# Performance work log

Measured on AMD Instinct MI355X. Metric: run time of the kernel, lower is better.

Reference implementation:

```python
import jax, jax.numpy as jnp
import numpy as np

N, M, IN, H, OUT, L = 100000, 50000, 256, 256, 128, 2
E_RAND = 150000  # extra random incidences beyond coverage prefixes
GN_STRUCT_EPS = float(H)  # GraphNorm(hidden, hidden): 2nd positional arg is eps!


def _l2n(a):
    return a / jnp.maximum(jnp.linalg.norm(a, axis=1, keepdims=True), 1e-12)


def _ln(x, g, b, eps=1e-5):
    m = x.mean(-1, keepdims=True)
    v = ((x - m) ** 2).mean(-1, keepdims=True)
    return (x - m) / jnp.sqrt(v + eps) * g + b


def _gn(x, w, b, ms, eps):
    # PyG GraphNorm with batch=None (single graph)
    mean = x.mean(0, keepdims=True)
    out = x - mean * ms
    var = (out ** 2).mean(0, keepdims=True)
    return w * out / jnp.sqrt(var + eps) + b


def _hgconv(xn, W, bias, src, dst, n_nodes, n_edges):
    # PyG HypergraphConv, use_attention=False -> heads=1, lin has no bias
    xw = xn @ W.T                                                # [n_nodes, H]
    ones = jnp.ones(src.shape[0], xw.dtype)
    Dn = jax.ops.segment_sum(ones, src, num_segments=n_nodes)   # node degree
    Dn = jnp.where(Dn > 0, 1.0 / Dn, 0.0)
    Be = jax.ops.segment_sum(ones, dst, num_segments=n_edges)   # hyperedge degree
    Be = jnp.where(Be > 0, 1.0 / Be, 0.0)
    he = jax.ops.segment_sum(xw[src], dst, num_segments=n_edges) * Be[:, None]
    out = jax.ops.segment_sum(he[dst], src, num_segments=n_nodes) * Dn[:, None]
    return out + bias


def _forward(x, x_e, x_struct_table, w_in, b_in, w_e, b_e, w_sem, b_sem,
             ln_n_g, ln_n_b, hg_w, hg_b,
             gn_struct_w, gn_struct_b, gn_struct_ms,
             gn_llm_w, gn_llm_b, gn_llm_ms,
             gn_d_w, gn_d_b, gn_d_ms,
             skip_w, skip_b,
             nf_ln1_g, nf_ln1_b, nf_w, nf_b, nf_ln2_g, nf_ln2_b,
             ef_ln1_g, ef_ln1_b, ef_w, ef_b, ef_ln2_g, ef_ln2_b,
             lin_w, lin_b, edge_index):
    lrelu = jax.nn.leaky_relu  # slope 0.01 == nn.LeakyReLU default
    src, dst = edge_index[0], edge_index[1]
    n, m = x.shape[0], x_e.shape[0]
    # edge_index[0] covers all nodes, so unique(edge_index[0]) == arange(N)
    xs = lrelu(_l2n(x_struct_table) @ w_in.T + b_in)   # dropout: eval mode (identity)
    xn = lrelu(_l2n(x) @ w_sem.T + b_sem)
    xe = lrelu(_l2n(x_e) @ w_e.T + b_e)
    for i in range(L):
        xs = _ln(xs, ln_n_g[i], ln_n_b[i])
        xs = lrelu(_hgconv(xs, hg_w[i, 0], hg_b[i, 0], src, dst, n, m)) + \
             _gn(xs, gn_struct_w[i], gn_struct_b[i], gn_struct_ms[i], GN_STRUCT_EPS)
        xn = _gn(xn, gn_llm_w[i], gn_llm_b[i], gn_llm_ms[i], 1e-5)
        xn = lrelu(_hgconv(xn, hg_w[i, 1], hg_b[i, 1], src, dst, n, m)) + \
             (xn @ skip_w[i, 0].T + skip_b[i, 0])
        agg = jax.ops.segment_min(xn[src], dst, num_segments=m)  # MinAggregation
        xe = _gn(xe + agg, gn_d_w[i], gn_d_b[i], gn_d_ms[i], 1e-5)
        # dual hypergraph: hyperedges become nodes (flip of edge_index)
        xe = lrelu(_hgconv(xe, hg_w[i, 2], hg_b[i, 2], dst, src, m, n)) + \
             (xe @ skip_w[i, 1].T + skip_b[i, 1])
    xf = jnp.concatenate([xs, xn], axis=1)
    xf = _ln(xf, nf_ln1_g, nf_ln1_b)
    xf = lrelu(xf @ nf_w.T + nf_b)
    xf = _ln(xf, nf_ln2_g, nf_ln2_b)
    xa = jax.ops.segment_min(xf[src], dst, num_segments=m)
    xef = jnp.concatenate([xa, xe], axis=1)
    xef = _ln(xef, ef_ln1_g, ef_ln1_b)
    xef = lrelu(xef @ ef_w.T + ef_b)
    xef = _ln(xef, ef_ln2_g, ef_ln2_b)
    return xef @ lin_w.T + lin_b  # [M, OUT]


def setup_inputs() -> dict:
    key = jax.random.key(0)
    ks = iter(jax.random.split(key, 64))
    def nrm(shape, scale=0.05):
        return jax.random.normal(next(ks), shape, dtype=jnp.float32) * scale
    # incidence list with guaranteed coverage of all nodes and all hyperedges
    src = jnp.concatenate([jnp.arange(N),
                           jax.random.randint(next(ks), (M + E_RAND,), 0, N)])
    dst = jnp.concatenate([jax.random.randint(next(ks), (N,), 0, M),
                           jnp.arange(M),
                           jax.random.randint(next(ks), (E_RAND,), 0, M)])
    edge_index = jnp.stack([src, dst]).astype(jnp.int32)  # [2, 300000]
    return dict(
        x=nrm((N, IN), 1.0), x_e=nrm((M, IN), 1.0), x_struct_table=nrm((N, IN), 1.0),
        w_in=nrm((H, IN)), b_in=jnp.zeros((H,)),
        w_e=nrm((H, IN)), b_e=jnp.zeros((H,)),
        w_sem=nrm((H, IN)), b_sem=jnp.zeros((H,)),
        ln_n_g=jnp.ones((L, H)), ln_n_b=jnp.zeros((L, H)),
        hg_w=nrm((L, 3, H, H)), hg_b=jnp.zeros((L, 3, H)),
        gn_struct_w=jnp.ones((L, H)), gn_struct_b=jnp.zeros((L, H)), gn_struct_ms=jnp.ones((L, H)),
        gn_llm_w=jnp.ones((L, H)), gn_llm_b=jnp.zeros((L, H)), gn_llm_ms=jnp.ones((L, H)),
        gn_d_w=jnp.ones((L, H)), gn_d_b=jnp.zeros((L, H)), gn_d_ms=jnp.ones((L, H)),
        skip_w=nrm((L, 2, H, H)), skip_b=jnp.zeros((L, 2, H)),
        nf_ln1_g=jnp.ones((2 * H,)), nf_ln1_b=jnp.zeros((2 * H,)),
        nf_w=nrm((H, 2 * H)), nf_b=jnp.zeros((H,)),
        nf_ln2_g=jnp.ones((H,)), nf_ln2_b=jnp.zeros((H,)),
        ef_ln1_g=jnp.ones((2 * H,)), ef_ln1_b=jnp.zeros((2 * H,)),
        ef_w=nrm((H, 2 * H)), ef_b=jnp.zeros((H,)),
        ef_ln2_g=jnp.ones((H,)), ef_ln2_b=jnp.zeros((H,)),
        lin_w=nrm((OUT, H)), lin_b=jnp.zeros((OUT,)),
        edge_index=edge_index,
    )


def reference(x, x_e, x_struct_table, w_in, b_in, w_e, b_e, w_sem, b_sem,
              ln_n_g, ln_n_b, hg_w, hg_b,
              gn_struct_w, gn_struct_b, gn_struct_ms,
              gn_llm_w, gn_llm_b, gn_llm_ms,
              gn_d_w, gn_d_b, gn_d_ms,
              skip_w, skip_b,
              nf_ln1_g, nf_ln1_b, nf_w, nf_b, nf_ln2_g, nf_ln2_b,
              ef_ln1_g, ef_ln1_b, ef_w, ef_b, ef_ln2_g, ef_ln2_b,
              lin_w, lin_b, edge_index):
    return _forward(x, x_e, x_struct_table, w_in, b_in, w_e, b_e, w_sem, b_sem,
                    ln_n_g, ln_n_b, hg_w, hg_b,
                    gn_struct_w, gn_struct_b, gn_struct_ms,
                    gn_llm_w, gn_llm_b, gn_llm_ms,
                    gn_d_w, gn_d_b, gn_d_ms,
                    skip_w, skip_b,
                    nf_ln1_g, nf_ln1_b, nf_w, nf_b, nf_ln2_g, nf_ln2_b,
                    ef_ln1_g, ef_ln1_b, ef_w, ef_b, ef_ln2_g, ef_ln2_b,
                    lin_w, lin_b, edge_index)
```

## Files before the change

kernel.cpp:

```cpp
#include <hip/hip_runtime.h>

typedef unsigned short u16;
struct __align__(16) us8 { ushort4 a, b; };
typedef __attribute__((ext_vector_type(8))) short bf16x8;
typedef __attribute__((ext_vector_type(4))) float f32x4;

#define CDIV(a,b) (((a)+(b)-1)/(b))

__device__ __forceinline__ float bf2f(u16 u){ return __uint_as_float(((unsigned)u)<<16); }
__device__ __forceinline__ u16 f2bf(float f){
  unsigned u=__float_as_uint(f);
  unsigned r=u+0x7fffu+((u>>16)&1u);
  return (u16)(r>>16);
}
__device__ __forceinline__ float lrelu_f(float v){ return v>0.f? v:0.01f*v; }
__device__ __forceinline__ float wsum(float v){
  #pragma unroll
  for(int o=32;o>0;o>>=1) v+=__shfl_xor(v,o,64);
  return v;
}
__device__ __forceinline__ void us8_to_f(const us8& v, float* f){
  f[0]=bf2f(v.a.x); f[1]=bf2f(v.a.y); f[2]=bf2f(v.a.z); f[3]=bf2f(v.a.w);
  f[4]=bf2f(v.b.x); f[5]=bf2f(v.b.y); f[6]=bf2f(v.b.z); f[7]=bf2f(v.b.w);
}
__device__ __forceinline__ us8 f_to_us8(const float* f){
  us8 v;
  v.a.x=f2bf(f[0]); v.a.y=f2bf(f[1]); v.a.z=f2bf(f[2]); v.a.w=f2bf(f[3]);
  v.b.x=f2bf(f[4]); v.b.y=f2bf(f[5]); v.b.z=f2bf(f[6]); v.b.w=f2bf(f[7]);
  return v;
}

__global__ void zero_k(unsigned* __restrict__ p, int n){
  int i=blockIdx.x*256+threadIdx.x; if(i<n) p[i]=0u;
}
__global__ void cvt_k(const float* __restrict__ in, u16* __restrict__ out, int n){
  int i = (blockIdx.x*256+threadIdx.x)*4;
  if(i+3<n){
    float4 v=*(const float4*)(in+i);
    ushort4 o; o.x=f2bf(v.x); o.y=f2bf(v.y); o.z=f2bf(v.z); o.w=f2bf(v.w);
    *(ushort4*)(out+i)=o;
  } else {
    for(int q=0;q<4&&i+q<n;q++) out[i+q]=f2bf(in[i+q]);
  }
}

__global__ void count_k(const int* __restrict__ src, const int* __restrict__ dst, int E,
                        int* __restrict__ cnt_src, int* __restrict__ cnt_dst){
  int e = blockIdx.x*256+threadIdx.x;
  if(e>=E) return;
  atomicAdd(&cnt_src[src[e]],1);
  atomicAdd(&cnt_dst[dst[e]],1);
}

#define SCAN_CHUNK 1024
__global__ void scan_pass1(const int* __restrict__ in, int n, int* __restrict__ partial){
  __shared__ int red[256];
  int base = blockIdx.x*SCAN_CHUNK;
  int s=0;
  for(int j=threadIdx.x;j<SCAN_CHUNK;j+=256){ int i=base+j; if(i<n) s+=in[i]; }
  red[threadIdx.x]=s; __syncthreads();
  for(int st=128;st>0;st>>=1){ if(threadIdx.x<st) red[threadIdx.x]+=red[threadIdx.x+st]; __syncthreads(); }
  if(threadIdx.x==0) partial[blockIdx.x]=red[0];
}
__global__ void scan_pass2(int* __restrict__ partial, int nb){
  __shared__ int buf[1024];
  for(int j=threadIdx.x;j<1024;j+=256) buf[j] = (j<nb)? partial[j]:0;
  __syncthreads();
  if(threadIdx.x==0){ int run=0; for(int j=0;j<nb;j++){ int v=buf[j]; buf[j]=run; run+=v; } }
  __syncthreads();
  for(int j=threadIdx.x;j<nb;j+=256) partial[j]=buf[j];
}
__global__ void scan_pass3(const int* __restrict__ in, int n, const int* __restrict__ partial,
                           int* __restrict__ out, int total){
  __shared__ int red[256];
  int base = blockIdx.x*SCAN_CHUNK;
  int j0 = base + threadIdx.x*4;
  int v[4]; int s=0;
  #pragma unroll
  for(int q=0;q<4;q++){ int i=j0+q; v[q]=(i<n)? in[i]:0; s+=v[q]; }
  red[threadIdx.x]=s; __syncthreads();
  if(threadIdx.x==0){ int run=0; for(int j=0;j<256;j++){ int t=red[j]; red[j]=run; run+=t; } }
  __syncthreads();
  int run = partial[blockIdx.x] + red[threadIdx.x];
  #pragma unroll
  for(int q=0;q<4;q++){ int i=j0+q; if(i<n) out[i]=run; run+=v[q]; }
  if(base==0 && threadIdx.x==0) out[n]=total;
}
__global__ void copy_int_k(const int* __restrict__ in, int* __restrict__ out, int n){
  int i=blockIdx.x*256+threadIdx.x;
  if(i<n) out[i]=in[i];
}
__global__ void fill_adj_k(const int* __restrict__ src, const int* __restrict__ dst, int E,
                           int* __restrict__ cur_src, int* __restrict__ cur_dst,
                           int* __restrict__ adj_sd, int* __restrict__ adj_ds){
  int e = blockIdx.x*256+threadIdx.x;
  if(e>=E) return;
  int s=src[e], d=dst[e];
  int p = atomicAdd(&cur_dst[d],1); adj_ds[p]=s;
  int q = atomicAdd(&cur_src[s],1); adj_sd[q]=d;
}
__global__ void invdeg_k(const int* __restrict__ off, float* __restrict__ inv, int S){
  int s=blockIdx.x*256+threadIdx.x;
  if(s>=S) return;
  int d=off[s+1]-off[s];
  inv[s] = d>0 ? 1.0f/(float)d : 0.0f;
}

__global__ void l2norm_k(const float* __restrict__ in, u16* __restrict__ out, int R){
  int r = blockIdx.x*4 + (threadIdx.x>>6);
  if(r>=R) return;
  int c = (threadIdx.x&63)*4;
  float4 v = *(const float4*)(in + (size_t)r*256 + c);
  float q = wsum(v.x*v.x+v.y*v.y+v.z*v.z+v.w*v.w);
  float sc = 1.0f/fmaxf(sqrtf(q),1e-12f);
  ushort4 o; o.x=f2bf(v.x*sc); o.y=f2bf(v.y*sc); o.z=f2bf(v.z*sc); o.w=f2bf(v.w*sc);
  *(ushort4*)(out + (size_t)r*256 + c) = o;
}

__global__ void ln_rows_k(u16* __restrict__ x, const float* __restrict__ g,
                          const float* __restrict__ b, int R){
  int r = blockIdx.x*4 + (threadIdx.x>>6);
  if(r>=R) return;
  int lane = threadIdx.x&63; int c = lane*4;
  u16* row = x + (size_t)r*256;
  ushort4 u = *(const ushort4*)(row + c);
  float v0=bf2f(u.x), v1=bf2f(u.y), v2=bf2f(u.z), v3=bf2f(u.w);
  float mean = wsum(v0+v1+v2+v3) * (1.f/256.f);
  float d0=v0-mean,d1=v1-mean,d2=v2-mean,d3=v3-mean;
  float var = wsum(d0*d0+d1*d1+d2*d2+d3*d3) * (1.f/256.f);
  float inv = 1.0f/sqrtf(var + 1e-5f);
  ushort4 ov;
  ov.x=f2bf(d0*inv*g[c+0]+b[c+0]);
  ov.y=f2bf(d1*inv*g[c+1]+b[c+1]);
  ov.z=f2bf(d2*inv*g[c+2]+b[c+2]);
  ov.w=f2bf(d3*inv*g[c+3]+b[c+3]);
  *(ushort4*)(row + c) = ov;
}

__global__ void ln512_k(u16* __restrict__ Lb, u16* __restrict__ Rb,
                        const float* __restrict__ g, const float* __restrict__ b, int R){
  int r = blockIdx.x*4 + (threadIdx.x>>6);
  if(r>=R) return;
  int lane = threadIdx.x&63; int c = lane*4;
  u16* rowL = Lb + (size_t)r*256;
  u16* rowR = Rb + (size_t)r*256;
  ushort4 ul = *(const ushort4*)(rowL + c);
  ushort4 ur = *(const ushort4*)(rowR + c);
  float l0=bf2f(ul.x), l1=bf2f(ul.y), l2=bf2f(ul.z), l3=bf2f(ul.w);
  float r0=bf2f(ur.x), r1=bf2f(ur.y), r2=bf2f(ur.z), r3=bf2f(ur.w);
  float mean = wsum(l0+l1+l2+l3+r0+r1+r2+r3) * (1.f/512.f);
  float a0=l0-mean,a1=l1-mean,a2=l2-mean,a3=l3-mean;
  float b0=r0-mean,b1=r1-mean,b2=r2-mean,b3=r3-mean;
  float var = wsum(a0*a0+a1*a1+a2*a2+a3*a3+b0*b0+b1*b1+b2*b2+b3*b3) * (1.f/512.f);
  float inv = 1.0f/sqrtf(var + 1e-5f);
  int cr = 256+c;
  ushort4 ovl, ovr;
  ovl.x=f2bf(a0*inv*g[c+0]+b[c+0]);
  ovl.y=f2bf(a1*inv*g[c+1]+b[c+1]);
  ovl.z=f2bf(a2*inv*g[c+2]+b[c+2]);
  ovl.w=f2bf(a3*inv*g[c+3]+b[c+3]);
  ovr.x=f2bf(b0*inv*g[cr+0]+b[cr+0]);
  ovr.y=f2bf(b1*inv*g[cr+1]+b[cr+1]);
  ovr.z=f2bf(b2*inv*g[cr+2]+b[cr+2]);
  ovr.w=f2bf(b3*inv*g[cr+3]+b[cr+3]);
  *(ushort4*)(rowL + c) = ovl;
  *(ushort4*)(rowR + c) = ovr;
}

__global__ void colstat_k(const u16* __restrict__ x, const u16* __restrict__ x2,
                          float* __restrict__ stat, int R){
  __shared__ float sh[512];
  int tid = threadIdx.x;
  for(int j=tid;j<512;j+=256) sh[j]=0.f;
  __syncthreads();
  int c = (tid&63)*4;
  float s0=0,s1=0,s2=0,s3=0,q0=0,q1=0,q2=0,q3=0;
  for(int r=blockIdx.x*4+(tid>>6); r<R; r+=gridDim.x*4){
    ushort4 u = *(const ushort4*)(x + (size_t)r*256 + c);
    float v0=bf2f(u.x), v1=bf2f(u.y), v2=bf2f(u.z), v3=bf2f(u.w);
    if(x2){
      ushort4 w = *(const ushort4*)(x2 + (size_t)r*256 + c);
      v0+=bf2f(w.x); v1+=bf2f(w.y); v2+=bf2f(w.z); v3+=bf2f(w.w);
    }
    s0+=v0; s1+=v1; s2+=v2; s3+=v3;
    q0+=v0*v0; q1+=v1*v1; q2+=v2*v2; q3+=v3*v3;
  }
  atomicAdd(&sh[c+0],s0); atomicAdd(&sh[c+1],s1);
  atomicAdd(&sh[c+2],s2); atomicAdd(&sh[c+3],s3);
  atomicAdd(&sh[256+c+0],q0); atomicAdd(&sh[256+c+1],q1);
  atomicAdd(&sh[256+c+2],q2); atomicAdd(&sh[256+c+3],q3);
  __syncthreads();
  for(int j=tid;j<512;j+=256) atomicAdd(&stat[j], sh[j]);
}
__global__ void gn_final_k(const float* __restrict__ stat, const float* __restrict__ w,
                           const float* __restrict__ b, const float* __restrict__ ms,
                           float eps, float invR,
                           float* __restrict__ gA, float* __restrict__ gS, float* __restrict__ gB){
  int c=threadIdx.x;
  float mean = stat[c]*invR;
  float a = mean*ms[c];
  float ex2 = stat[256+c]*invR;
  float var = ex2 - 2.f*a*mean + a*a;
  gA[c]=a;
  gS[c]=w[c]/sqrtf(var+eps);
  gB[c]=b[c];
}
__global__ void apply_gn_k(u16* __restrict__ x, const u16* __restrict__ add,
                           const float* __restrict__ gA, const float* __restrict__ gS,
                           const float* __restrict__ gB, size_t n4){
  size_t stride = (size_t)gridDim.x*256;
  for(size_t p=(size_t)blockIdx.x*256+threadIdx.x; p<n4; p+=stride){
    int c = (int)(p&63)*4;
    ushort4 u = ((const ushort4*)x)[p];
    float v0=bf2f(u.x), v1=bf2f(u.y), v2=bf2f(u.z), v3=bf2f(u.w);
    if(add){
      ushort4 a = ((const ushort4*)add)[p];
      v0+=bf2f(a.x); v1+=bf2f(a.y); v2+=bf2f(a.z); v3+=bf2f(a.w);
    }
    v0 = fmaf(gS[c+0], v0-gA[c+0], gB[c+0]);
    v1 = fmaf(gS[c+1], v1-gA[c+1], gB[c+1]);
    v2 = fmaf(gS[c+2], v2-gA[c+2], gB[c+2]);
    v3 = fmaf(gS[c+3], v3-gA[c+3], gB[c+3]);
    ushort4 o; o.x=f2bf(v0); o.y=f2bf(v1); o.z=f2bf(v2); o.w=f2bf(v3);
    ((ushort4*)x)[p]=o;
  }
}

template<int MODE>
__global__ void seg_sum_k(const u16* __restrict__ in, u16* __restrict__ out,
    const int* __restrict__ adj, const int* __restrict__ off,
    const float* __restrict__ inv, const float* __restrict__ bias,
    const u16* __restrict__ resid,
    const float* __restrict__ gA, const float* __restrict__ gS, const float* __restrict__ gB,
    int S){
  int s = blockIdx.x*8 + (threadIdx.x>>5);
  if(s>=S) return;
  int c = (threadIdx.x&31)*8;
  int jb=off[s], je=off[s+1];
  float a[8]={0.f,0.f,0.f,0.f,0.f,0.f,0.f,0.f};
  for(int j=jb;j<je;j++){
    us8 v = *(const us8*)(in + (size_t)adj[j]*256 + c);
    float f[8]; us8_to_f(v,f);
    #pragma unroll
    for(int q=0;q<8;q++) a[q]+=f[q];
  }
  float sc = inv[s];
  float o[8];
  if(MODE==0){
    #pragma unroll
    for(int q=0;q<8;q++) o[q]=a[q]*sc;
  } else {
    #pragma unroll
    for(int q=0;q<8;q++) o[q] = lrelu_f(fmaf(a[q],sc,bias[c+q]));
    us8 p = *(const us8*)(resid + (size_t)s*256 + c);
    float pf[8]; us8_to_f(p,pf);
    if(MODE==1){
      #pragma unroll
      for(int q=0;q<8;q++) o[q] += fmaf(gS[c+q], pf[q]-gA[c+q], gB[c+q]);
    } else {
      #pragma unroll
      for(int q=0;q<8;q++) o[q] += pf[q];
    }
  }
  *(us8*)(out + (size_t)s*256 + c) = f_to_us8(o);
}

__global__ void seg_min_k(const u16* __restrict__ in, u16* __restrict__ out,
    const int* __restrict__ adj, const int* __restrict__ off, int S){
  int s = blockIdx.x*8 + (threadIdx.x>>5);
  if(s>=S) return;
  int c = (threadIdx.x&31)*8;
  int jb=off[s], je=off[s+1];
  float m[8];
  #pragma unroll
  for(int q=0;q<8;q++) m[q]=3.402823466e38f;
  for(int j=jb;j<je;j++){
    us8 v = *(const us8*)(in + (size_t)adj[j]*256 + c);
    float f[8]; us8_to_f(v,f);
    #pragma unroll
    for(int q=0;q<8;q++) m[q]=fminf(m[q],f[q]);
  }
  if(jb==je){
    #pragma unroll
    for(int q=0;q<8;q++) m[q]=0.f;
  }
  *(us8*)(out + (size_t)s*256 + c) = f_to_us8(m);
}

template<int FLAGS, int JT>
__global__ __launch_bounds__(512, 3)
void gemm_mfma(const u16* A0, const u16* __restrict__ A1,
               const u16* __restrict__ Wb, const float* __restrict__ bias,
               u16* Cb, float* __restrict__ Cf, int R, int K){
  const int CN = JT*64;
  __shared__ u16 sm[64*(JT*64+8)];
  const int t = threadIdx.x;
  const int row0 = blockIdx.x*128;
  const int lane = t&63;
  const int w = t>>6;
  const int wrow = (w>>2)*64, wcol = (w&3)*(JT*16);
  const int lm = lane&15, q = lane>>4;
  f32x4 acc[4][4];
  #pragma unroll
  for(int i=0;i<4;i++)
    #pragma unroll
    for(int j=0;j<JT;j++) acc[i][j] = (f32x4){0.f,0.f,0.f,0.f};

  int arow[4];
  #pragma unroll
  for(int i=0;i<4;i++){
    int r = row0 + wrow + i*16 + lm;
    arow[i] = r < R ? r : (R-1);
  }
  const u16* brow[JT];
  #pragma unroll
  for(int j=0;j<JT;j++) brow[j] = Wb + (size_t)(wcol + j*16 + lm)*K + q*8;

  #pragma unroll 2
  for(int kt=0; kt<K; kt+=32){
    const u16* Ab = ((FLAGS&8) && kt>=256) ? A1 : A0;
    const int kc = (kt & 255) + q*8;
    bf16x8 af[4], bfv[4];
    #pragma unroll
    for(int i=0;i<4;i++)  af[i]  = *(const bf16x8*)(Ab + (size_t)arow[i]*256 + kc);
    #pragma unroll
    for(int j=0;j<JT;j++) bfv[j] = *(const bf16x8*)(brow[j] + kt);
    #pragma unroll
    for(int i=0;i<4;i++)
      #pragma unroll
      for(int j=0;j<JT;j++)
        acc[i][j] = __builtin_amdgcn_mfma_f32_16x16x32_bf16(af[i], bfv[j], acc[i][j], 0,0,0);
  }

  float bvals[4];
  #pragma unroll
  for(int j=0;j<JT;j++) bvals[j] = (FLAGS&1) ? bias[wcol+j*16+lm] : 0.f;

  if(FLAGS&4){
    #pragma unroll
    for(int j=0;j<JT;j++){
      int col = wcol + j*16 + lm;
      #pragma unroll
      for(int i=0;i<4;i++){
        int rbase = row0 + wrow + i*16 + q*4;
        #pragma unroll
        for(int rg=0;rg<4;rg++){
          int r = rbase+rg;
          if(r>=R) continue;
          float v = acc[i][j][rg] + bvals[j];
          if(FLAGS&2) v = lrelu_f(v);
          Cf[(size_t)r*CN+col] = v;
        }
      }
    }
  } else {
    const int CEPI = CN+8;
    const int ROWU = CN/8;
    #pragma unroll
    for(int h=0; h<2; h++){
      if((w>>2)==h){
        #pragma unroll
        for(int j=0;j<JT;j++){
          int cl = wcol + j*16 + lm;
          #pragma unroll
          for(int i=0;i<4;i++){
            #pragma unroll
            for(int rg=0;rg<4;rg++){
              float v = acc[i][j][rg] + bvals[j];
              if(FLAGS&2) v = lrelu_f(v);
              sm[(i*16 + q*4 + rg)*CEPI + cl] = f2bf(v);
            }
          }
        }
      }
      __syncthreads();
      #pragma unroll
      for(int it=0; it<64*ROWU/512; it++){
        int idx = it*512 + t;
        int rl = idx/ROWU, c8 = (idx - rl*ROWU)*8;
        int r = row0 + h*64 + rl;
        if(r<R) *(us8*)(Cb + (size_t)r*CN + c8) = *(const us8*)(&sm[rl*CEPI + c8]);
      }
      __syncthreads();
    }
  }
}

extern "C" void kernel_launch(void* const* d_in, const int* in_sizes, int n_in,
                              void* d_out, int out_size, void* d_ws, size_t ws_size,
                              hipStream_t stream){
  const int H = 256;
  const int N = in_sizes[0]/H;
  const int M = in_sizes[1]/H;
  const int E = in_sizes[38]/2;

  const float* x     = (const float*)d_in[0];
  const float* x_e   = (const float*)d_in[1];
  const float* x_st  = (const float*)d_in[2];
  const float* w_in  = (const float*)d_in[3];  const float* b_in  = (const float*)d_in[4];
  const float* w_e   = (const float*)d_in[5];  const float* b_e   = (const float*)d_in[6];
  const float* w_sem = (const float*)d_in[7];  const float* b_sem = (const float*)d_in[8];
  const float* ln_n_g = (const float*)d_in[9]; const float* ln_n_b = (const float*)d_in[10];
  const float* hg_w  = (const float*)d_in[11]; const float* hg_b  = (const float*)d_in[12];
  const float* gns_w = (const float*)d_in[13]; const float* gns_b = (const float*)d_in[14]; const float* gns_ms = (const float*)d_in[15];
  const float* gnl_w = (const float*)d_in[16]; const float* gnl_b = (const float*)d_in[17]; const float* gnl_ms = (const float*)d_in[18];
  const float* gnd_w = (const float*)d_in[19]; const float* gnd_b = (const float*)d_in[20]; const float* gnd_ms = (const float*)d_in[21];
  const float* skip_w = (const float*)d_in[22]; const float* skip_b = (const float*)d_in[23];
  const float* nf_ln1_g = (const float*)d_in[24]; const float* nf_ln1_b = (const float*)d_in[25];
  const float* nf_w = (const float*)d_in[26]; const float* nf_b = (const float*)d_in[27];
  const float* nf_ln2_g = (const float*)d_in[28]; const float* nf_ln2_b = (const float*)d_in[29];
  const float* ef_ln1_g = (const float*)d_in[30]; const float* ef_ln1_b = (const float*)d_in[31];
  const float* ef_w = (const float*)d_in[32]; const float* ef_b = (const float*)d_in[33];
  const float* ef_ln2_g = (const float*)d_in[34]; const float* ef_ln2_b = (const float*)d_in[35];
  const float* lin_w = (const float*)d_in[36]; const float* lin_b = (const float*)d_in[37];
  const int* edge = (const int*)d_in[38];
  const int* src = edge;
  const int* dst = edge + E;
  float* outp = (float*)d_out;

  const size_t NH=(size_t)N*H, MH=(size_t)M*H;
  u16* XS = (u16*)d_ws;
  u16* XN = XS + NH;
  u16* TN = XN + NH;
  u16* XE = TN + NH;
  u16* TM = XE + MH;
  float* dinv = (float*)(TM + MH);
  float* binv = dinv + N;
  float* stat = binv + M;
  float* gA = stat+512; float* gS = gA+256; float* gB = gS+256;
  int* cnt_src = (int*)(gB+256);
  int* cnt_dst = cnt_src + N;
  int* off_src = cnt_dst + M;
  int* off_dst = off_src + (N+1);
  int* adj_ds = off_dst + (M+1);
  int* adj_sd = adj_ds + E;
  int* partial = adj_sd + E;
  u16* wb = (u16*)(((uintptr_t)(partial+1024)+15)&~(uintptr_t)15);
  u16* wb_in  = wb;
  u16* wb_sem = wb_in  + 65536;
  u16* wb_e   = wb_sem + 65536;
  u16* wb_hg  = wb_e   + 65536;
  u16* wb_sk  = wb_hg  + 6*65536;
  u16* wb_nf  = wb_sk  + 4*65536;
  u16* wb_ef  = wb_nf  + 131072;
  u16* wb_lin = wb_ef  + 131072;

  cvt_k<<<CDIV(65536,1024),256,0,stream>>>(w_in, wb_in, 65536);
  cvt_k<<<CDIV(65536,1024),256,0,stream>>>(w_sem, wb_sem, 65536);
  cvt_k<<<CDIV(65536,1024),256,0,stream>>>(w_e, wb_e, 65536);
  cvt_k<<<CDIV(6*65536,1024),256,0,stream>>>(hg_w, wb_hg, 6*65536);
  cvt_k<<<CDIV(4*65536,1024),256,0,stream>>>(skip_w, wb_sk, 4*65536);
  cvt_k<<<CDIV(131072,1024),256,0,stream>>>(nf_w, wb_nf, 131072);
  cvt_k<<<CDIV(131072,1024),256,0,stream>>>(ef_w, wb_ef, 131072);
  cvt_k<<<CDIV(32768,1024),256,0,stream>>>(lin_w, wb_lin, 32768);

  zero_k<<<CDIV(N+M,256),256,0,stream>>>((unsigned*)cnt_src, N+M);
  count_k<<<CDIV(E,256),256,0,stream>>>(src,dst,E,cnt_src,cnt_dst);
  int nbN = CDIV(N,SCAN_CHUNK), nbM = CDIV(M,SCAN_CHUNK);
  scan_pass1<<<nbN,256,0,stream>>>(cnt_src,N,partial);
  scan_pass2<<<1,256,0,stream>>>(partial,nbN);
  scan_pass3<<<nbN,256,0,stream>>>(cnt_src,N,partial,off_src,E);
  scan_pass1<<<nbM,256,0,stream>>>(cnt_dst,M,partial);
  scan_pass2<<<1,256,0,stream>>>(partial,nbM);
  scan_pass3<<<nbM,256,0,stream>>>(cnt_dst,M,partial,off_dst,E);
  copy_int_k<<<CDIV(N,256),256,0,stream>>>(off_src,cnt_src,N);
  copy_int_k<<<CDIV(M,256),256,0,stream>>>(off_dst,cnt_dst,M);
  fill_adj_k<<<CDIV(E,256),256,0,stream>>>(src,dst,E,cnt_src,cnt_dst,adj_sd,adj_ds);
  invdeg_k<<<CDIV(N,256),256,0,stream>>>(off_src,dinv,N);
  invdeg_k<<<CDIV(M,256),256,0,stream>>>(off_dst,binv,M);

  auto gemm = [&](int F, const u16* A0, const u16* A1, const u16* Wt, const float* bias,
                  u16* Cb, float* Cf, int R, int K){
    dim3 g(CDIV(R,128));
    switch(F){
      case 0:  gemm_mfma<0,4> <<<g,512,0,stream>>>(A0,A1,Wt,bias,Cb,Cf,R,K); break;
      case 1:  gemm_mfma<1,4> <<<g,512,0,stream>>>(A0,A1,Wt,bias,Cb,Cf,R,K); break;
      case 3:  gemm_mfma<3,4> <<<g,512,0,stream>>>(A0,A1,Wt,bias,Cb,Cf,R,K); break;
      case 5:  gemm_mfma<5,2> <<<g,512,0,stream>>>(A0,A1,Wt,bias,Cb,Cf,R,K); break;
      case 11: gemm_mfma<11,4><<<g,512,0,stream>>>(A0,A1,Wt,bias,Cb,Cf,R,K); break;
    }
  };
  auto colstats = [&](const u16* xx, const u16* x2, const float* w, const float* b,
                      const float* ms, float eps, int R){
    zero_k<<<2,256,0,stream>>>((unsigned*)stat, 512);
    colstat_k<<<256,256,0,stream>>>(xx, x2, stat, R);
    gn_final_k<<<1,256,0,stream>>>(stat, w, b, ms, eps, 1.0f/(float)R, gA,gS,gB);
  };

  l2norm_k<<<CDIV(N,4),256,0,stream>>>(x_st, TN, N);
  gemm(3, TN, nullptr, wb_in, b_in, XS, nullptr, N, 256);
  l2norm_k<<<CDIV(N,4),256,0,stream>>>(x, TN, N);
  gemm(3, TN, nullptr, wb_sem, b_sem, XN, nullptr, N, 256);
  l2norm_k<<<CDIV(M,4),256,0,stream>>>(x_e, TM, M);
  gemm(3, TM, nullptr, wb_e, b_e, XE, nullptr, M, 256);

  for(int i=0;i<2;i++){
    ln_rows_k<<<CDIV(N,4),256,0,stream>>>(XS, ln_n_g+i*H, ln_n_b+i*H, N);
    colstats(XS, nullptr, gns_w+i*H, gns_b+i*H, gns_ms+i*H, 256.0f, N);
    seg_sum_k<0><<<CDIV(M,8),256,0,stream>>>(XS, TM, adj_ds, off_dst, binv, nullptr,nullptr,nullptr,nullptr,nullptr, M);
    gemm(0, TM, nullptr, wb_hg+(size_t)(i*3+0)*65536, nullptr, TM, nullptr, M, 256);
    seg_sum_k<1><<<CDIV(N,8),256,0,stream>>>(TM, XS, adj_sd, off_src, dinv, hg_b+(size_t)(i*3+0)*H, XS, gA,gS,gB, N);

    colstats(XN, nullptr, gnl_w+i*H, gnl_b+i*H, gnl_ms+i*H, 1e-5f, N);
    apply_gn_k<<<1024,256,0,stream>>>(XN, nullptr, gA,gS,gB, NH/4);
    seg_sum_k<0><<<CDIV(M,8),256,0,stream>>>(XN, TM, adj_ds, off_dst, binv, nullptr,nullptr,nullptr,nullptr,nullptr, M);
    gemm(0, TM, nullptr, wb_hg+(size_t)(i*3+1)*65536, nullptr, TM, nullptr, M, 256);
    gemm(1, XN, nullptr, wb_sk+(size_t)(i*2+0)*65536, skip_b+(size_t)(i*2+0)*H, TN, nullptr, N, 256);
    seg_sum_k<2><<<CDIV(N,8),256,0,stream>>>(TM, XN, adj_sd, off_src, dinv, hg_b+(size_t)(i*3+1)*H, TN, nullptr,nullptr,nullptr, N);

    seg_min_k<<<CDIV(M,8),256,0,stream>>>(XN, TM, adj_ds, off_dst, M);
    colstats(XE, TM, gnd_w+i*H, gnd_b+i*H, gnd_ms+i*H, 1e-5f, M);
    apply_gn_k<<<1024,256,0,stream>>>(XE, TM, gA,gS,gB, MH/4);
    gemm(0, XE, nullptr, wb_hg+(size_t)(i*3+2)*65536, nullptr, TM, nullptr, M, 256);
    seg_sum_k<0><<<CDIV(N,8),256,0,stream>>>(TM, TN, adj_sd, off_src, dinv, nullptr,nullptr,nullptr,nullptr,nullptr, N);
    gemm(1, XE, nullptr, wb_sk+(size_t)(i*2+1)*65536, skip_b+(size_t)(i*2+1)*H, TM, nullptr, M, 256);
    seg_sum_k<2><<<CDIV(M,8),256,0,stream>>>(TN, XE, adj_ds, off_dst, binv, hg_b+(size_t)(i*3+2)*H, TM, nullptr,nullptr,nullptr, M);
  }

  ln512_k<<<CDIV(N,4),256,0,stream>>>(XS, XN, nf_ln1_g, nf_ln1_b, N);
  gemm(11, XS, XN, wb_nf, nf_b, TN, nullptr, N, 512);
  ln_rows_k<<<CDIV(N,4),256,0,stream>>>(TN, nf_ln2_g, nf_ln2_b, N);
  seg_min_k<<<CDIV(M,8),256,0,stream>>>(TN, TM, adj_ds, off_dst, M);
  ln512_k<<<CDIV(M,4),256,0,stream>>>(TM, XE, ef_ln1_g, ef_ln1_b, M);
  gemm(11, TM, XE, wb_ef, ef_b, XS, nullptr, M, 512);
  ln_rows_k<<<CDIV(M,4),256,0,stream>>>(XS, ef_ln2_g, ef_ln2_b, M);
  gemm(5, XS, nullptr, wb_lin, lin_b, nullptr, outp, M, 256);
}
```

Before: 2.163 ms.

## Stage GEMM A tile into swizzled LDS shared across waves

The MFMA GEMM now cooperatively loads the block's 128x256 A tile into shared memory once per K-phase, using an XOR swizzle to avoid bank conflicts. Waves then read their A fragments from LDS instead of each column-wave re-fetching the same rows from global memory. B fragments are still read straight from global. The larger 64KB shared allocation and the added barriers may reduce occupancy and serialize loading against compute.

```diff
diff --git a/kernel.cpp b/kernel.cpp
--- a/kernel.cpp
+++ b/kernel.cpp
@@ -293,7 +293,8 @@
                const u16* __restrict__ Wb, const float* __restrict__ bias,
                u16* Cb, float* __restrict__ Cf, int R, int K){
   const int CN = JT*64;
-  __shared__ u16 sm[64*(JT*64+8)];
+  __shared__ u16 sm[128*256];
+  u16* As = sm;
   const int t = threadIdx.x;
   const int row0 = blockIdx.x*128;
   const int lane = t&63;
@@ -306,30 +307,50 @@
     #pragma unroll
     for(int j=0;j<JT;j++) acc[i][j] = (f32x4){0.f,0.f,0.f,0.f};
 
-  int arow[4];
-  #pragma unroll
-  for(int i=0;i<4;i++){
-    int r = row0 + wrow + i*16 + lm;
-    arow[i] = r < R ? r : (R-1);
-  }
   const u16* brow[JT];
   #pragma unroll
   for(int j=0;j<JT;j++) brow[j] = Wb + (size_t)(wcol + j*16 + lm)*K + q*8;
 
-  #pragma unroll 2
-  for(int kt=0; kt<K; kt+=32){
-    const u16* Ab = ((FLAGS&8) && kt>=256) ? A1 : A0;
-    const int kc = (kt & 255) + q*8;
-    bf16x8 af[4], bfv[4];
-    #pragma unroll
-    for(int i=0;i<4;i++)  af[i]  = *(const bf16x8*)(Ab + (size_t)arow[i]*256 + kc);
-    #pragma unroll
-    for(int j=0;j<JT;j++) bfv[j] = *(const bf16x8*)(brow[j] + kt);
-    #pragma unroll
-    for(int i=0;i<4;i++)
-      #pragma unroll
-      for(int j=0;j<JT;j++)
-        acc[i][j] = __builtin_amdgcn_mfma_f32_16x16x32_bf16(af[i], bfv[j], acc[i][j], 0,0,0);
+  auto stage = [&](const u16* Ab){
+    #pragma unroll
+    for(int h=0; h<2; h++){
+      us8 sv[4];
+      #pragma unroll
+      for(int p=0;p<4;p++){
+        int idx = (h*4+p)*512 + t;
+        int row = idx>>5, ch = idx&31;
+        int rg = row0+row; rg = rg<R ? rg : (R-1);
+        sv[p] = *(const us8*)(Ab + (size_t)rg*256 + ch*8);
+      }
+      #pragma unroll
+      for(int p=0;p<4;p++){
+        int idx = (h*4+p)*512 + t;
+        int row = idx>>5, ch = idx&31;
+        *(us8*)(&As[row*256 + ((ch^(row&7))<<3)]) = sv[p];
+      }
+    }
+    __syncthreads();
+  };
+
+  const int nph = (FLAGS&8) ? 2 : 1;
+  for(int ph=0; ph<nph; ph++){
+    stage(ph ? A1 : A0);
+    const int kb = ph<<8;
+    #pragma unroll 2
+    for(int st=0; st<8; st++){
+      bf16x8 af[4], bfv[4];
+      #pragma unroll
+      for(int j=0;j<JT;j++) bfv[j] = *(const bf16x8*)(brow[j] + kb + st*32);
+      #pragma unroll
+      for(int i=0;i<4;i++)
+        af[i] = *(const bf16x8*)(&As[(wrow + i*16 + lm)*256 + ((((st<<2)+q)^(lm&7))<<3)]);
+      #pragma unroll
+      for(int i=0;i<4;i++)
+        #pragma unroll
+        for(int j=0;j<JT;j++)
+          acc[i][j] = __builtin_amdgcn_mfma_f32_16x16x32_bf16(af[i], bfv[j], acc[i][j], 0,0,0);
+    }
+    __syncthreads();
   }
 
   float bvals[4];
```

After: 2.020 ms. 1.07x faster.
